# Kernel optimization log

Measured on AMD Instinct MI355X. Metric: run time of the kernel, lower is better.

Reference implementation:

```python
import jax, jax.numpy as jnp
import numpy as np

NNZ = 524288
IN_FEATURES = 50000
OUT_FEATURES = 512
N_ROWS = 4096


def setup_inputs() -> dict:
    key = jax.random.key(0)
    k1, k2, k3, k4, k5 = jax.random.split(key, 5)
    values = jax.random.normal(k1, (NNZ,), dtype=jnp.float32)
    weight = jax.random.normal(k2, (IN_FEATURES, OUT_FEATURES), dtype=jnp.float32)
    bias = jax.random.normal(k3, (OUT_FEATURES,), dtype=jnp.float32)
    rows = jax.random.randint(k4, (NNZ,), 0, N_ROWS)
    cols = jax.random.randint(k5, (NNZ,), 0, IN_FEATURES)
    return {
        "values": values,
        "weight": weight,
        "bias": bias,
        "rows": rows,
        "cols": cols,
        "n_rows": N_ROWS,
    }


def reference(values, weight, bias, rows, cols, n_rows):
    # SpMM: out[r, :] = sum_{k: rows[k]==r} values[k] * weight[cols[k], :]
    contrib = values[:, None] * weight[cols]               # [nnz, out]
    out = jax.ops.segment_sum(contrib, rows, num_segments=n_rows)  # [n_rows, out]
    return out + bias
```

## Files before the change

### kernel.cpp

```cpp
#include <hip/hip_runtime.h>
#include <hip/hip_fp16.h>


__global__ void convert_count_kernel(const float* __restrict__ weight,
                                     __half* __restrict__ wf16, long long ngroups,
                                     const int* __restrict__ rows,
                                     int* __restrict__ counts, int nnz) {
    long long i = (long long)blockIdx.x * blockDim.x + threadIdx.x;
    if (i < nnz) atomicAdd(&counts[rows[(int)i]], 1);
    const float4* w4 = (const float4*)weight;
    float4* dst = (float4*)wf16;
    long long stride = (long long)gridDim.x * blockDim.x;
    for (long long g = i; g < ngroups; g += stride) {
        float4 a = w4[2 * g];
        float4 b = w4[2 * g + 1];
        union { __half2 h2[4]; float4 f4; } u;
        u.h2[0] = __floats2half2_rn(a.x, a.y);
        u.h2[1] = __floats2half2_rn(a.z, a.w);
        u.h2[2] = __floats2half2_rn(b.x, b.y);
        u.h2[3] = __floats2half2_rn(b.z, b.w);
        dst[g] = u.f4;
    }
}

__global__ void scan_kernel(const int* __restrict__ counts, int* __restrict__ offsets,
                            int* __restrict__ cursor, int n_rows) {
    __shared__ int partial[256];
    const int t = threadIdx.x;
    const int per = (n_rows + 255) / 256;
    const int base = t * per;
    int sum = 0;
    for (int j = 0; j < per; ++j) {
        int idx = base + j;
        if (idx < n_rows) sum += counts[idx];
    }
    partial[t] = sum;
    __syncthreads();
    for (int off = 1; off < 256; off <<= 1) {
        int v = 0;
        if (t >= off) v = partial[t - off];
        __syncthreads();
        if (t >= off) partial[t] += v;
        __syncthreads();
    }
    int run = (t == 0) ? 0 : partial[t - 1];
    for (int j = 0; j < per; ++j) {
        int idx = base + j;
        if (idx < n_rows) {
            offsets[idx] = run;
            cursor[idx] = run;
            run += counts[idx];
        }
    }
    if (t == 255) offsets[n_rows] = run;
}

__global__ void scatter_pairs_kernel(const int* __restrict__ rows, const int* __restrict__ cols,
                                     const float* __restrict__ values, int* __restrict__ cursor,
                                     int2* __restrict__ pairs, int nnz) {
    int i = blockIdx.x * blockDim.x + threadIdx.x;
    if (i < nnz) {
        int p = atomicAdd(&cursor[rows[i]], 1);
        pairs[p] = make_int2(cols[i], __float_as_int(values[i]));
    }
}

__global__ __launch_bounds__(256) void sort_rows_kernel(const int* __restrict__ offsets,
                                                        int2* __restrict__ pairs) {
    const int row = blockIdx.x;
    const int start = offsets[row];
    const int n = offsets[row + 1] - start;
    if (n > 256) return;
    __shared__ unsigned long long key[256];
    const int t = threadIdx.x;
    if (t < n) {
        int2 e = pairs[start + t];
        key[t] = ((unsigned long long)(unsigned)e.x << 32) | (unsigned)e.y;
    } else {
        key[t] = ~0ull;
    }
    for (int k = 2; k <= 256; k <<= 1) {
        for (int j = k >> 1; j > 0; j >>= 1) {
            __syncthreads();
            int l = t ^ j;
            if (l > t) {
                unsigned long long a = key[t];
                unsigned long long b = key[l];
                bool asc = (t & k) == 0;
                if (asc ? (a > b) : (a < b)) {
                    key[t] = b;
                    key[l] = a;
                }
            }
        }
    }
    __syncthreads();
    if (t < n) {
        pairs[start + t] = make_int2((int)(key[t] >> 32),
                                     (int)(unsigned)(key[t] & 0xffffffffull));
    }
}

__global__ __launch_bounds__(256) void accum_f16_kernel(
    const __half* __restrict__ wf16, const float* __restrict__ bias,
    const int* __restrict__ offsets, const int2* __restrict__ pairs,
    float* __restrict__ out, int out_f) {
    const int wave = threadIdx.x >> 6;
    const int lane = threadIdx.x & 63;
    const int half = blockIdx.x & 1;
    const int row = (blockIdx.x >> 1) * 4 + wave;
    const int start = offsets[row];
    const int end   = offsets[row + 1];

    const int colbase = half * 256 + lane * 4;
    const float2* wbase = (const float2*)wf16;
    const int fidx = colbase >> 2;
    const int frow = out_f >> 2;

    float acc0 = 0.f, acc1 = 0.f, acc2 = 0.f, acc3 = 0.f;

    int p = start;
    for (; p + 4 <= end; p += 4) {
        int2 e0 = pairs[p];
        int2 e1 = pairs[p + 1];
        int2 e2 = pairs[p + 2];
        int2 e3 = pairs[p + 3];
        float2 w0 = wbase[(long long)e0.x * frow + fidx];
        float2 w1 = wbase[(long long)e1.x * frow + fidx];
        float2 w2 = wbase[(long long)e2.x * frow + fidx];
        float2 w3 = wbase[(long long)e3.x * frow + fidx];
        float v0 = __int_as_float(e0.y);
        float v1 = __int_as_float(e1.y);
        float v2 = __int_as_float(e2.y);
        float v3 = __int_as_float(e3.y);
        {
            const __half2* h = (const __half2*)&w0;
            float2 a = __half22float2(h[0]), b = __half22float2(h[1]);
            acc0 += v0 * a.x; acc1 += v0 * a.y; acc2 += v0 * b.x; acc3 += v0 * b.y;
        }
        {
            const __half2* h = (const __half2*)&w1;
            float2 a = __half22float2(h[0]), b = __half22float2(h[1]);
            acc0 += v1 * a.x; acc1 += v1 * a.y; acc2 += v1 * b.x; acc3 += v1 * b.y;
        }
        {
            const __half2* h = (const __half2*)&w2;
            float2 a = __half22float2(h[0]), b = __half22float2(h[1]);
            acc0 += v2 * a.x; acc1 += v2 * a.y; acc2 += v2 * b.x; acc3 += v2 * b.y;
        }
        {
            const __half2* h = (const __half2*)&w3;
            float2 a = __half22float2(h[0]), b = __half22float2(h[1]);
            acc0 += v3 * a.x; acc1 += v3 * a.y; acc2 += v3 * b.x; acc3 += v3 * b.y;
        }
    }
    for (; p < end; ++p) {
        int2 e0 = pairs[p];
        float v0 = __int_as_float(e0.y);
        float2 w0 = wbase[(long long)e0.x * frow + fidx];
        const __half2* h = (const __half2*)&w0;
        float2 a = __half22float2(h[0]), b = __half22float2(h[1]);
        acc0 += v0 * a.x; acc1 += v0 * a.y; acc2 += v0 * b.x; acc3 += v0 * b.y;
    }

    float4 bv = *(const float4*)(bias + colbase);
    float4 o = make_float4(acc0 + bv.x, acc1 + bv.y, acc2 + bv.z, acc3 + bv.w);
    *(float4*)(out + (long long)row * out_f + colbase) = o;
}

__global__ void count_rows_kernel(const int* __restrict__ rows, int* __restrict__ counts, int nnz) {
    int i = blockIdx.x * blockDim.x + threadIdx.x;
    if (i < nnz) atomicAdd(&counts[rows[i]], 1);
}
__global__ void scatter_kernel(const int* __restrict__ rows, int* __restrict__ cursor,
                               int* __restrict__ perm, int nnz) {
    int i = blockIdx.x * blockDim.x + threadIdx.x;
    if (i < nnz) {
        int p = atomicAdd(&cursor[rows[i]], 1);
        perm[p] = i;
    }
}
__global__ void accum_kernel(const float* __restrict__ values, const float* __restrict__ weight,
                             const float* __restrict__ bias, const int* __restrict__ cols,
                             const int* __restrict__ offsets, const int* __restrict__ perm,
                             float* __restrict__ out, int out_f) {
    const int r = blockIdx.x;
    const int start = offsets[r];
    const int end = offsets[r + 1];
    const int step = blockDim.x * 4;
    for (int base = threadIdx.x * 4; base < out_f; base += step) {
        float4 acc = make_float4(0.f, 0.f, 0.f, 0.f);
        for (int p = start; p < end; ++p) {
            int k = perm[p];
            float v = values[k];
            long long c = cols[k];
            float4 w = *(const float4*)(weight + c * (long long)out_f + base);
            acc.x += v * w.x; acc.y += v * w.y; acc.z += v * w.z; acc.w += v * w.w;
        }
        float4 b = *(const float4*)(bias + base);
        acc.x += b.x; acc.y += b.y; acc.z += b.z; acc.w += b.w;
        *(float4*)(out + (long long)r * out_f + base) = acc;
    }
}

static size_t align_up(size_t x, size_t a) { return (x + a - 1) & ~(a - 1); }

extern "C" void kernel_launch(void* const* d_in, const int* in_sizes, int n_in,
                              void* d_out, int out_size, void* d_ws, size_t ws_size,
                              hipStream_t stream) {
    const float* values = (const float*)d_in[0];
    const float* weight = (const float*)d_in[1];
    const float* bias   = (const float*)d_in[2];
    const int*   rows   = (const int*)d_in[3];
    const int*   cols   = (const int*)d_in[4];

    const int nnz = in_sizes[0];
    const long long wtotal = in_sizes[1];
    const int out_f = in_sizes[2];
    const int n_rows = out_size / out_f;
    float* out = (float*)d_out;

    size_t off_wf16 = 0;
    size_t off_counts = align_up(off_wf16 + (size_t)wtotal * sizeof(__half), 256);
    size_t off_offsets = off_counts + (size_t)n_rows * sizeof(int);
    size_t off_cursor = off_offsets + (size_t)(n_rows + 1) * sizeof(int);
    size_t off_pairs = align_up(off_cursor + (size_t)n_rows * sizeof(int), 256);
    size_t need = off_pairs + (size_t)nnz * sizeof(int2);

    if (ws_size >= need && out_f == 512 && (n_rows % 4) == 0) {
        char* ws = (char*)d_ws;
        __half* wf16 = (__half*)(ws + off_wf16);
        int* counts = (int*)(ws + off_counts);
        int* offsets = (int*)(ws + off_offsets);
        int* cursor = (int*)(ws + off_cursor);
        int2* pairs = (int2*)(ws + off_pairs);

        hipMemsetAsync(counts, 0, (size_t)n_rows * sizeof(int), stream);

        long long ngroups = wtotal / 8;
        int cc_blocks = (int)((ngroups + 255) / 256);
        convert_count_kernel<<<cc_blocks, 256, 0, stream>>>(weight, wf16, ngroups,
                                                            rows, counts, nnz);
        scan_kernel<<<1, 256, 0, stream>>>(counts, offsets, cursor, n_rows);
        int sc_blocks = (nnz + 255) / 256;
        scatter_pairs_kernel<<<sc_blocks, 256, 0, stream>>>(rows, cols, values, cursor,
                                                            pairs, nnz);
        sort_rows_kernel<<<n_rows, 256, 0, stream>>>(offsets, pairs);
        accum_f16_kernel<<<(n_rows / 4) * 2, 256, 0, stream>>>(wf16, bias, offsets, pairs,
                                                               out, out_f);
    } else {
        int* counts = (int*)d_ws;
        int* offsets = counts + n_rows;
        int* cursor = offsets + n_rows + 1;
        int* perm = cursor + n_rows;
        hipMemsetAsync(counts, 0, (size_t)n_rows * sizeof(int), stream);
        int blocks = (nnz + 255) / 256;
        count_rows_kernel<<<blocks, 256, 0, stream>>>(rows, counts, nnz);
        scan_kernel<<<1, 256, 0, stream>>>(counts, offsets, cursor, n_rows);
        scatter_kernel<<<blocks, 256, 0, stream>>>(rows, cursor, perm, nnz);
        accum_kernel<<<n_rows, 128, 0, stream>>>(values, weight, bias, cols,
                                                 offsets, perm, out, out_f);
    }
}
```

Baseline: 330.4 us.

## Drop fp16 weight conversion and gather fp32 weights directly in accumulation

Removes the per-call pass that converts the whole 50000x512 fp32 weight matrix to fp16, and instead gathers fp32 weight rows directly in the accumulate kernel. Each block now covers a quarter of the output columns with float2 per lane, and the inner loop is unrolled 8-wide to keep more gathers in flight. This avoids reading ~100MB and writing ~50MB per call, but doubles the bytes fetched per gathered weight row in the accumulation and launches twice as many blocks.

```diff
diff --git a/kernel.cpp b/kernel.cpp
--- a/kernel.cpp
+++ b/kernel.cpp
@@ -2,25 +2,9 @@
 #include <hip/hip_fp16.h>
 
 
-__global__ void convert_count_kernel(const float* __restrict__ weight,
-                                     __half* __restrict__ wf16, long long ngroups,
-                                     const int* __restrict__ rows,
-                                     int* __restrict__ counts, int nnz) {
-    long long i = (long long)blockIdx.x * blockDim.x + threadIdx.x;
-    if (i < nnz) atomicAdd(&counts[rows[(int)i]], 1);
-    const float4* w4 = (const float4*)weight;
-    float4* dst = (float4*)wf16;
-    long long stride = (long long)gridDim.x * blockDim.x;
-    for (long long g = i; g < ngroups; g += stride) {
-        float4 a = w4[2 * g];
-        float4 b = w4[2 * g + 1];
-        union { __half2 h2[4]; float4 f4; } u;
-        u.h2[0] = __floats2half2_rn(a.x, a.y);
-        u.h2[1] = __floats2half2_rn(a.z, a.w);
-        u.h2[2] = __floats2half2_rn(b.x, b.y);
-        u.h2[3] = __floats2half2_rn(b.z, b.w);
-        dst[g] = u.f4;
-    }
+__global__ void count_rows_kernel(const int* __restrict__ rows, int* __restrict__ counts, int nnz) {
+    int i = blockIdx.x * blockDim.x + threadIdx.x;
+    if (i < nnz) atomicAdd(&counts[rows[i]], 1);
 }
 
 __global__ void scan_kernel(const int* __restrict__ counts, int* __restrict__ offsets,
@@ -101,77 +85,54 @@
     }
 }
 
-__global__ __launch_bounds__(256) void accum_f16_kernel(
-    const __half* __restrict__ wf16, const float* __restrict__ bias,
+__global__ __launch_bounds__(256) void accum_f32_kernel(
+    const float* __restrict__ weight, const float* __restrict__ bias,
     const int* __restrict__ offsets, const int2* __restrict__ pairs,
     float* __restrict__ out, int out_f) {
     const int wave = threadIdx.x >> 6;
     const int lane = threadIdx.x & 63;
-    const int half = blockIdx.x & 1;
-    const int row = (blockIdx.x >> 1) * 4 + wave;
+    const int quarter = blockIdx.x & 3;
+    const int row = (blockIdx.x >> 2) * 4 + wave;
     const int start = offsets[row];
     const int end   = offsets[row + 1];
 
-    const int colbase = half * 256 + lane * 4;
-    const float2* wbase = (const float2*)wf16;
-    const int fidx = colbase >> 2;
-    const int frow = out_f >> 2;
-
-    float acc0 = 0.f, acc1 = 0.f, acc2 = 0.f, acc3 = 0.f;
-
+    const int colbase = quarter * 128 + lane * 2;
+    const float2* wbase = (const float2*)weight;
+    const int fidx = colbase >> 1;
+    const int frow = out_f >> 1;
+
+    float acc0 = 0.f, acc1 = 0.f;
+
+    constexpr int U = 8;
     int p = start;
-    for (; p + 4 <= end; p += 4) {
-        int2 e0 = pairs[p];
-        int2 e1 = pairs[p + 1];
-        int2 e2 = pairs[p + 2];
-        int2 e3 = pairs[p + 3];
-        float2 w0 = wbase[(long long)e0.x * frow + fidx];
-        float2 w1 = wbase[(long long)e1.x * frow + fidx];
-        float2 w2 = wbase[(long long)e2.x * frow + fidx];
-        float2 w3 = wbase[(long long)e3.x * frow + fidx];
-        float v0 = __int_as_float(e0.y);
-        float v1 = __int_as_float(e1.y);
-        float v2 = __int_as_float(e2.y);
-        float v3 = __int_as_float(e3.y);
-        {
-            const __half2* h = (const __half2*)&w0;
-            float2 a = __half22float2(h[0]), b = __half22float2(h[1]);
-            acc0 += v0 * a.x; acc1 += v0 * a.y; acc2 += v0 * b.x; acc3 += v0 * b.y;
-        }
-        {
-            const __half2* h = (const __half2*)&w1;
-            float2 a = __half22float2(h[0]), b = __half22float2(h[1]);
-            acc0 += v1 * a.x; acc1 += v1 * a.y; acc2 += v1 * b.x; acc3 += v1 * b.y;
-        }
-        {
-            const __half2* h = (const __half2*)&w2;
-            float2 a = __half22float2(h[0]), b = __half22float2(h[1]);
-            acc0 += v2 * a.x; acc1 += v2 * a.y; acc2 += v2 * b.x; acc3 += v2 * b.y;
-        }
-        {
-            const __half2* h = (const __half2*)&w3;
-            float2 a = __half22float2(h[0]), b = __half22float2(h[1]);
-            acc0 += v3 * a.x; acc1 += v3 * a.y; acc2 += v3 * b.x; acc3 += v3 * b.y;
+    for (; p + U <= end; p += U) {
+        int2 e[U];
+#pragma unroll
+        for (int u = 0; u < U; ++u) e[u] = pairs[p + u];
+        float2 w[U];
+#pragma unroll
+        for (int u = 0; u < U; ++u)
+            w[u] = wbase[(long long)e[u].x * frow + fidx];
+#pragma unroll
+        for (int u = 0; u < U; ++u) {
+            float v = __int_as_float(e[u].y);
+            acc0 += v * w[u].x;
+            acc1 += v * w[u].y;
         }
     }
     for (; p < end; ++p) {
         int2 e0 = pairs[p];
         float v0 = __int_as_float(e0.y);
         float2 w0 = wbase[(long long)e0.x * frow + fidx];
-        const __half2* h = (const __half2*)&w0;
-        float2 a = __half22float2(h[0]), b = __half22float2(h[1]);
-        acc0 += v0 * a.x; acc1 += v0 * a.y; acc2 += v0 * b.x; acc3 += v0 * b.y;
-    }
-
-    float4 bv = *(const float4*)(bias + colbase);
-    float4 o = make_float4(acc0 + bv.x, acc1 + bv.y, acc2 + bv.z, acc3 + bv.w);
-    *(float4*)(out + (long long)row * out_f + colbase) = o;
-}
-
-__global__ void count_rows_kernel(const int* __restrict__ rows, int* __restrict__ counts, int nnz) {
-    int i = blockIdx.x * blockDim.x + threadIdx.x;
-    if (i < nnz) atomicAdd(&counts[rows[i]], 1);
-}
+        acc0 += v0 * w0.x;
+        acc1 += v0 * w0.y;
+    }
+
+    float2 bv = *(const float2*)(bias + colbase);
+    float2 o = make_float2(acc0 + bv.x, acc1 + bv.y);
+    *(float2*)(out + (long long)row * out_f + colbase) = o;
+}
+
 __global__ void scatter_kernel(const int* __restrict__ rows, int* __restrict__ cursor,
                                int* __restrict__ perm, int nnz) {
     int i = blockIdx.x * blockDim.x + threadIdx.x;
@@ -215,13 +176,11 @@
     const int*   cols   = (const int*)d_in[4];
 
     const int nnz = in_sizes[0];
-    const long long wtotal = in_sizes[1];
     const int out_f = in_sizes[2];
     const int n_rows = out_size / out_f;
     float* out = (float*)d_out;
 
-    size_t off_wf16 = 0;
-    size_t off_counts = align_up(off_wf16 + (size_t)wtotal * sizeof(__half), 256);
+    size_t off_counts = 0;
     size_t off_offsets = off_counts + (size_t)n_rows * sizeof(int);
     size_t off_cursor = off_offsets + (size_t)(n_rows + 1) * sizeof(int);
     size_t off_pairs = align_up(off_cursor + (size_t)n_rows * sizeof(int), 256);
@@ -229,7 +188,6 @@
 
     if (ws_size >= need && out_f == 512 && (n_rows % 4) == 0) {
         char* ws = (char*)d_ws;
-        __half* wf16 = (__half*)(ws + off_wf16);
         int* counts = (int*)(ws + off_counts);
         int* offsets = (int*)(ws + off_offsets);
         int* cursor = (int*)(ws + off_cursor);
@@ -237,17 +195,14 @@
 
         hipMemsetAsync(counts, 0, (size_t)n_rows * sizeof(int), stream);
 
-        long long ngroups = wtotal / 8;
-        int cc_blocks = (int)((ngroups + 255) / 256);
-        convert_count_kernel<<<cc_blocks, 256, 0, stream>>>(weight, wf16, ngroups,
-                                                            rows, counts, nnz);
+        int blocks = (nnz + 255) / 256;
+        count_rows_kernel<<<blocks, 256, 0, stream>>>(rows, counts, nnz);
         scan_kernel<<<1, 256, 0, stream>>>(counts, offsets, cursor, n_rows);
-        int sc_blocks = (nnz + 255) / 256;
-        scatter_pairs_kernel<<<sc_blocks, 256, 0, stream>>>(rows, cols, values, cursor,
-                                                            pairs, nnz);
+        scatter_pairs_kernel<<<blocks, 256, 0, stream>>>(rows, cols, values, cursor,
+                                                         pairs, nnz);
         sort_rows_kernel<<<n_rows, 256, 0, stream>>>(offsets, pairs);
-        accum_f16_kernel<<<(n_rows / 4) * 2, 256, 0, stream>>>(wf16, bias, offsets, pairs,
-                                                               out, out_f);
+        accum_f32_kernel<<<(n_rows / 4) * 4, 256, 0, stream>>>(weight, bias, offsets,
+                                                               pairs, out, out_f);
     } else {
         int* counts = (int*)d_ws;
         int* offsets = counts + n_rows;
```

New measurement: 377.8 us. 14.3% more time.
